# Kernel tuning notes

Hardware: AMD Instinct MI355X
Metric: run time of the kernel (lower is better)

## Reference

```python
import jax, jax.numpy as jnp
import numpy as np

C = 6.5  # ALCOVE specificity constant

BATCH, NE, NDIMS = 2048, 2048, 128


def setup_inputs() -> dict:
    key = jax.random.key(0)
    k1, k2, k3 = jax.random.split(key, 3)
    inputs = jax.random.normal(k1, (BATCH, NDIMS), dtype=jnp.float32)
    exemplars = jax.random.normal(k2, (NE, NDIMS), dtype=jnp.float32)
    # attn initialized to ones/ndims in the original; use positive random values
    # scaled similarly so the exp argument stays in a reasonable range.
    attn = jax.random.uniform(k3, (NDIMS,), dtype=jnp.float32) / float(NDIMS)
    return {"inputs": inputs, "exemplars": exemplars, "attn": attn}


def reference(inputs, exemplars, attn):
    # Vectorized form of: exp(-c * sum_d attn_d * |exemplars - x|) per example.
    # diff: (batch, ne, ndims)
    diff = jnp.abs(exemplars[None, :, :] - inputs[:, None, :])
    dist = jnp.einsum('bed,d->be', diff, attn)  # weighted L1 distance
    return jnp.exp(-C * dist)  # (batch, ne)
```

## Files before the change

### kernel.cpp

```cpp
#include <hip/hip_runtime.h>
#include <stdint.h>


#define BATCH 2048
#define NE 2048
#define ND 128

#define TB 64
#define TE 64
#define ND2 64

#define QSCALE 524288.0f
#define QBIAS  32768.5f
#define K2 (-6.5f * 1.4426950408889634f / 524288.0f)

#define SAD16(acc, a, b) asm("v_sad_u16 %0, %1, %2, %0" : "+v"(acc) : "v"(a), "v"(b))

typedef float vfloat4 __attribute__((ext_vector_type(4)));

__global__ __launch_bounds__(256, 4)
void alcove_rbf_kernel(const float* __restrict__ X,
                       const float* __restrict__ E,
                       const float* __restrict__ A,
                       float* __restrict__ out) {
  __shared__ uint32_t Xs[ND2 * TB];
  __shared__ uint32_t Es[ND2 * TE];

  const int tid = (int)threadIdx.x;

  const int bid = (int)blockIdx.y * 32 + (int)blockIdx.x;
  const int swz = (bid & 7) * 128 + (bid >> 3);
  const int e0 = (swz & 31) * TE;
  const int b0 = (swz >> 5) * TB;

  const int tx = tid & 15;
  const int ty = tid >> 4;
  const int lane_in = tid & 3;
  const int srow = tid >> 2;

  uint32_t acc[4][4];
#pragma unroll
  for (int j = 0; j < 4; ++j)
#pragma unroll
    for (int i = 0; i < 4; ++i) acc[j][i] = 0u;

  const float4* A4 = (const float4*)A;
#pragma unroll
  for (int it = 0; it < 8; ++it) {
    const int c4 = 4 * it + lane_in;
    const float4 a = A4[c4];
    const float sx = a.x * QSCALE, sy = a.y * QSCALE,
                sz = a.z * QSCALE, sw = a.w * QSCALE;
    const float4 vx = *(const float4*)(X + (size_t)(b0 + srow) * ND + 4 * c4);
    const float4 ve = *(const float4*)(E + (size_t)(e0 + srow) * ND + 4 * c4);

    const uint32_t x0 = ((uint32_t)fmaf(vx.x, sx, QBIAS)) |
                        (((uint32_t)fmaf(vx.y, sy, QBIAS)) << 16);
    const uint32_t x1 = ((uint32_t)fmaf(vx.z, sz, QBIAS)) |
                        (((uint32_t)fmaf(vx.w, sw, QBIAS)) << 16);
    const uint32_t e0w = ((uint32_t)fmaf(ve.x, sx, QBIAS)) |
                         (((uint32_t)fmaf(ve.y, sy, QBIAS)) << 16);
    const uint32_t e1w = ((uint32_t)fmaf(ve.z, sz, QBIAS)) |
                         (((uint32_t)fmaf(ve.w, sw, QBIAS)) << 16);

    Xs[(2 * c4 + 0) * TB + srow] = x0;
    Xs[(2 * c4 + 1) * TB + srow] = x1;
    Es[(2 * c4 + 0) * TE + srow] = e0w;
    Es[(2 * c4 + 1) * TE + srow] = e1w;
  }
  __syncthreads();

  const uint4* Xs4 = (const uint4*)Xs;
  const uint4* Es4 = (const uint4*)Es;
#pragma unroll 8
  for (int d2 = 0; d2 < ND2; ++d2) {
    const uint4 xv = Xs4[d2 * (TB / 4) + ty];
    const uint4 ev = Es4[d2 * (TE / 4) + tx];
    SAD16(acc[0][0], xv.x, ev.x); SAD16(acc[0][1], xv.x, ev.y);
    SAD16(acc[0][2], xv.x, ev.z); SAD16(acc[0][3], xv.x, ev.w);
    SAD16(acc[1][0], xv.y, ev.x); SAD16(acc[1][1], xv.y, ev.y);
    SAD16(acc[1][2], xv.y, ev.z); SAD16(acc[1][3], xv.y, ev.w);
    SAD16(acc[2][0], xv.z, ev.x); SAD16(acc[2][1], xv.z, ev.y);
    SAD16(acc[2][2], xv.z, ev.z); SAD16(acc[2][3], xv.z, ev.w);
    SAD16(acc[3][0], xv.w, ev.x); SAD16(acc[3][1], xv.w, ev.y);
    SAD16(acc[3][2], xv.w, ev.z); SAD16(acc[3][3], xv.w, ev.w);
  }

#pragma unroll
  for (int j = 0; j < 4; ++j) {
    const int b = b0 + 4 * ty + j;
    vfloat4 o;
    o.x = exp2f(K2 * (float)acc[j][0]);
    o.y = exp2f(K2 * (float)acc[j][1]);
    o.z = exp2f(K2 * (float)acc[j][2]);
    o.w = exp2f(K2 * (float)acc[j][3]);
    vfloat4* dst = reinterpret_cast<vfloat4*>(out + (size_t)b * NE + e0) + tx;
    __builtin_nontemporal_store(o, dst);
  }
}

extern "C" void kernel_launch(void* const* d_in, const int* in_sizes, int n_in,
                              void* d_out, int out_size, void* d_ws, size_t ws_size,
                              hipStream_t stream) {
  const float* X = (const float*)d_in[0];
  const float* E = (const float*)d_in[1];
  const float* A = (const float*)d_in[2];
  float* out = (float*)d_out;

  dim3 grid(NE / TE, BATCH / TB);
  dim3 block(256);
  alcove_rbf_kernel<<<grid, block, 0, stream>>>(X, E, A, out);
}
```

Baseline: 73.36 us.

## Broadcast X operands via DPP row broadcast instead of per-step LDS loads

Reorganizes the X tile in shared memory with a rotated (bank-skewed) layout so each lane loads four uint4 words of X once into registers. In the main loop each row's X values are then broadcast across the 16 lanes of a DPP row with mov_dpp row_bcast, so only the E operand is read from LDS per step. This roughly halves LDS read traffic in the inner loop, at the cost of four DPP moves per iteration and a fully unrolled 64-step body that raises register pressure and code size.

```diff
diff --git a/kernel.cpp b/kernel.cpp
--- a/kernel.cpp
+++ b/kernel.cpp
@@ -16,7 +16,32 @@
 
 #define SAD16(acc, a, b) asm("v_sad_u16 %0, %1, %2, %0" : "+v"(acc) : "v"(a), "v"(b))
 
+#define RBC(v, t) \
+  ((uint32_t)__builtin_amdgcn_mov_dpp((int)(v), 0x150 + (t), 0xF, 0xF, false))
+
 typedef float vfloat4 __attribute__((ext_vector_type(4)));
+
+#define IT(K, T)                                                          \
+  {                                                                       \
+    const uint4 ev = Es4[(16 * (K) + (T)) * (TE / 4) + tx];               \
+    const uint32_t r0 = RBC(Xr[K].x, T);                                  \
+    const uint32_t r1 = RBC(Xr[K].y, T);                                  \
+    const uint32_t r2 = RBC(Xr[K].z, T);                                  \
+    const uint32_t r3 = RBC(Xr[K].w, T);                                  \
+    SAD16(acc[0][0], r0, ev.x); SAD16(acc[0][1], r0, ev.y);               \
+    SAD16(acc[0][2], r0, ev.z); SAD16(acc[0][3], r0, ev.w);               \
+    SAD16(acc[1][0], r1, ev.x); SAD16(acc[1][1], r1, ev.y);               \
+    SAD16(acc[1][2], r1, ev.z); SAD16(acc[1][3], r1, ev.w);               \
+    SAD16(acc[2][0], r2, ev.x); SAD16(acc[2][1], r2, ev.y);               \
+    SAD16(acc[2][2], r2, ev.z); SAD16(acc[2][3], r2, ev.w);               \
+    SAD16(acc[3][0], r3, ev.x); SAD16(acc[3][1], r3, ev.y);               \
+    SAD16(acc[3][2], r3, ev.z); SAD16(acc[3][3], r3, ev.w);               \
+  }
+
+#define IT16(K)                                                           \
+  IT(K, 0)  IT(K, 1)  IT(K, 2)  IT(K, 3)  IT(K, 4)  IT(K, 5)  IT(K, 6)   \
+  IT(K, 7)  IT(K, 8)  IT(K, 9)  IT(K, 10) IT(K, 11) IT(K, 12) IT(K, 13)  \
+  IT(K, 14) IT(K, 15)
 
 __global__ __launch_bounds__(256, 4)
 void alcove_rbf_kernel(const float* __restrict__ X,
@@ -63,28 +88,23 @@
     const uint32_t e1w = ((uint32_t)fmaf(ve.z, sz, QBIAS)) |
                          (((uint32_t)fmaf(ve.w, sw, QBIAS)) << 16);
 
-    Xs[(2 * c4 + 0) * TB + srow] = x0;
-    Xs[(2 * c4 + 1) * TB + srow] = x1;
-    Es[(2 * c4 + 0) * TE + srow] = e0w;
-    Es[(2 * c4 + 1) * TE + srow] = e1w;
+    const int d2a = 2 * c4, d2b = 2 * c4 + 1;
+    const int tyq = srow >> 2, rlo = srow & 3;
+    Xs[4 * (d2a * 16 + ((tyq + d2a) & 15)) + rlo] = x0;
+    Xs[4 * (d2b * 16 + ((tyq + d2b) & 15)) + rlo] = x1;
+    Es[d2a * TE + srow] = e0w;
+    Es[d2b * TE + srow] = e1w;
   }
   __syncthreads();
 
   const uint4* Xs4 = (const uint4*)Xs;
   const uint4* Es4 = (const uint4*)Es;
-#pragma unroll 8
-  for (int d2 = 0; d2 < ND2; ++d2) {
-    const uint4 xv = Xs4[d2 * (TB / 4) + ty];
-    const uint4 ev = Es4[d2 * (TE / 4) + tx];
-    SAD16(acc[0][0], xv.x, ev.x); SAD16(acc[0][1], xv.x, ev.y);
-    SAD16(acc[0][2], xv.x, ev.z); SAD16(acc[0][3], xv.x, ev.w);
-    SAD16(acc[1][0], xv.y, ev.x); SAD16(acc[1][1], xv.y, ev.y);
-    SAD16(acc[1][2], xv.y, ev.z); SAD16(acc[1][3], xv.y, ev.w);
-    SAD16(acc[2][0], xv.z, ev.x); SAD16(acc[2][1], xv.z, ev.y);
-    SAD16(acc[2][2], xv.z, ev.z); SAD16(acc[2][3], xv.z, ev.w);
-    SAD16(acc[3][0], xv.w, ev.x); SAD16(acc[3][1], xv.w, ev.y);
-    SAD16(acc[3][2], xv.w, ev.z); SAD16(acc[3][3], xv.w, ev.w);
-  }
+  uint4 Xr[4];
+#pragma unroll
+  for (int k = 0; k < 4; ++k)
+    Xr[k] = Xs4[(16 * k + tx) * 16 + ((ty + tx) & 15)];
+
+  IT16(0) IT16(1) IT16(2) IT16(3)
 
 #pragma unroll
   for (int j = 0; j < 4; ++j) {
```

Result: no change. 74.63 us (+1.7%).
